# Kernel tuning notes

Measured on AMD Instinct MI355X. Metric: run time of the kernel, lower is better.

## Reference

```python
import jax, jax.numpy as jnp
import numpy as np

S, D, H, MLP = 2048, 1024, 16, 4096
DK = D // H
EPS = 1e-5  # torch LayerNorm default


def setup_inputs() -> dict:
    key = jax.random.key(0)
    ks = jax.random.split(key, 8)
    init = lambda k, shape, fan_in: jax.random.normal(k, shape, jnp.float32) * (fan_in ** -0.5)
    return {
        "x": jax.random.normal(ks[0], (S, D), jnp.float32),
        "wq": init(ks[1], (D, D), D), "bq": jnp.zeros((D,), jnp.float32),
        "wk": init(ks[2], (D, D), D), "bk": jnp.zeros((D,), jnp.float32),
        "wv": init(ks[3], (D, D), D), "bv": jnp.zeros((D,), jnp.float32),
        "wo": init(ks[4], (D, D), D), "bo": jnp.zeros((D,), jnp.float32),
        "w1": init(ks[5], (D, MLP), D), "b1": jnp.zeros((MLP,), jnp.float32),
        "w2": init(ks[6], (MLP, D), MLP), "b2": jnp.zeros((D,), jnp.float32),
        "ln1_g": jnp.ones((D,), jnp.float32), "ln1_b": jnp.zeros((D,), jnp.float32),
        "ln2_g": jnp.ones((D,), jnp.float32), "ln2_b": jnp.zeros((D,), jnp.float32),
    }


def _layernorm(x, g, b):
    m = jnp.mean(x, axis=-1, keepdims=True)
    v = jnp.var(x, axis=-1, keepdims=True)
    return (x - m) * jax.lax.rsqrt(v + EPS) * g + b


def reference(x, wq, bq, wk, bk, wv, bv, wo, bo, w1, b1, w2, b2, ln1_g, ln1_b, ln2_g, ln2_b):
    # --- residual 1: pre-LN multi-head self-attention ---
    h = _layernorm(x, ln1_g, ln1_b)
    q = (h @ wq + bq).reshape(S, H, DK).transpose(1, 0, 2)  # [H,S,DK]
    k = (h @ wk + bk).reshape(S, H, DK).transpose(1, 0, 2)
    v = (h @ wv + bv).reshape(S, H, DK).transpose(1, 0, 2)
    scores = jnp.einsum('hqd,hkd->hqk', q, k) / jnp.sqrt(jnp.float32(DK))  # [H,S,S]
    attn = jax.nn.softmax(scores, axis=-1)
    o = jnp.einsum('hqk,hkd->hqd', attn, v)  # [H,S,DK]
    # Faithful to original: x.contiguous().view(S, -1) is a raw reshape of the
    # [H,S,DK] buffer (no transpose back to [S,H,DK]).
    o = o.reshape(S, D)
    x = x + (o @ wo + bo)
    # --- residual 2: pre-LN GELU FFN ---
    h2 = _layernorm(x, ln2_g, ln2_b)
    f = jax.nn.gelu(h2 @ w1 + b1, approximate=False)  # torch nn.GELU = exact erf
    x = x + (f @ w2 + b2)
    return x
```

## Files before the change

kernel.cpp:

```cpp
#include <hip/hip_runtime.h>


constexpr int kS = 2048, kD = 1024, kH = 16, kDK = 64, kMLP = 4096;
constexpr float kEps = 1e-5f;

using u16 = unsigned short;
using u32 = unsigned int;
typedef float f32x4 __attribute__((ext_vector_type(4)));
typedef short bf16x8 __attribute__((ext_vector_type(8)));

__device__ __forceinline__ u16 f2b(float f) {
  u32 u = __builtin_bit_cast(u32, f);
  return (u16)((u + 0x7fffu + ((u >> 16) & 1u)) >> 16);
}

typedef const __attribute__((address_space(1))) u32* gas1;
typedef __attribute__((address_space(3))) u32* las3;
__device__ __forceinline__ void async16(const void* g, void* l) {
  __builtin_amdgcn_global_load_lds((gas1)g, (las3)l, 16, 0, 0);
}

__global__ __launch_bounds__(256)
void ln_kernel(const float* __restrict__ x, const float* __restrict__ g,
               const float* __restrict__ b, u16* __restrict__ out) {
  __shared__ float red[8];
  const int row = blockIdx.x, tid = threadIdx.x;
  const float4 v = *(const float4*)(x + (size_t)row * kD + tid * 4);
  float s = v.x + v.y + v.z + v.w;
  float ss = v.x * v.x + v.y * v.y + v.z * v.z + v.w * v.w;
#pragma unroll
  for (int d = 1; d < 64; d <<= 1) { s += __shfl_xor(s, d); ss += __shfl_xor(ss, d); }
  if ((tid & 63) == 0) { red[tid >> 6] = s; red[4 + (tid >> 6)] = ss; }
  __syncthreads();
  const float m = (red[0] + red[1] + red[2] + red[3]) * (1.f / kD);
  const float var = (red[4] + red[5] + red[6] + red[7]) * (1.f / kD) - m * m;
  const float r = rsqrtf(var + kEps);
  const float4 gv = *(const float4*)(g + tid * 4);
  const float4 bv = *(const float4*)(b + tid * 4);
  ushort4 o;
  o.x = f2b((v.x - m) * r * gv.x + bv.x);
  o.y = f2b((v.y - m) * r * gv.y + bv.y);
  o.z = f2b((v.z - m) * r * gv.z + bv.z);
  o.w = f2b((v.w - m) * r * gv.w + bv.w);
  *(ushort4*)(out + (size_t)row * kD + tid * 4) = o;
}

__global__ __launch_bounds__(256)
void transpose_cvt(const float* __restrict__ in, u16* __restrict__ out, int R, int C) {
  __shared__ float tile[32][33];
  const int c0 = blockIdx.x * 32, r0 = blockIdx.y * 32;
  const int x = threadIdx.x, y = threadIdx.y;
#pragma unroll
  for (int i = 0; i < 4; ++i)
    tile[y + i * 8][x] = in[(size_t)(r0 + y + i * 8) * C + c0 + x];
  __syncthreads();
#pragma unroll
  for (int i = 0; i < 4; ++i)
    out[(size_t)(c0 + y + i * 8) * R + r0 + x] = f2b(tile[x][y + i * 8]);
}

__global__ void concat_bias(const float* __restrict__ bq, const float* __restrict__ bk,
                            const float* __restrict__ bv, float* __restrict__ out) {
  int i = blockIdx.x * 256 + threadIdx.x;
  out[i] = i < kD ? bq[i] : (i < 2 * kD ? bk[i - kD] : bv[i - 2 * kD]);
}

__global__ __launch_bounds__(256)
void vtrans(const u16* __restrict__ qkv, u16* __restrict__ vt) {
  __shared__ u16 t[64][72];
  const int s0 = blockIdx.x * 64, h = blockIdx.y, tid = threadIdx.x;
#pragma unroll
  for (int r = 0; r < 2; ++r) {
    int chunk = r * 256 + tid, row = chunk >> 3, col = (chunk & 7) * 8;
    uint4 v = *(const uint4*)(qkv + (size_t)(s0 + row) * 3072 + 2 * kD + h * 64 + col);
    *(uint4*)(&t[row][col]) = v;
  }
  __syncthreads();
#pragma unroll
  for (int r = 0; r < 2; ++r) {
    int chunk = r * 256 + tid, drow = chunk >> 3, scol = (chunk & 7) * 8;
    u16 tmp[8];
#pragma unroll
    for (int j = 0; j < 8; ++j) tmp[j] = t[scol + j][drow];
    *(uint4*)(vt + (size_t)h * 64 * kS + (size_t)drow * kS + s0 + scol) = *(uint4*)tmp;
  }
}

template <int EPI>
__global__ __launch_bounds__(256, 2)
void gemm_bt(const u16* __restrict__ A, const u16* __restrict__ Bt,
             const float* __restrict__ bias, void* __restrict__ Cout,
             int N, int K, int Ksub) {
  constexpr int BM = 128, BN = 128, BK = 32;
  constexpr int MT = 4, NT = 4;
  __shared__ u16 As[BM * BK];
  __shared__ u16 Bs[BN * BK];
  const int tid = threadIdx.x;
  const int w = tid >> 6, l = tid & 63;
  const int wm = w >> 1, wn = w & 1;
  const int row0 = blockIdx.y * BM, col0 = blockIdx.x * BN;
  const int koff = blockIdx.z * Ksub;

  const int sc = ((l & 3) ^ ((l >> 3) & 3)) * 8;
  const u16* Ag = A + (size_t)(row0 + w * 16 + (l >> 2)) * K + koff + sc;
  const u16* Bg = Bt + (size_t)(col0 + w * 16 + (l >> 2)) * K + koff + sc;
  u16* AsW = As + w * 512;
  u16* BsW = Bs + w * 512;

  f32x4 acc[MT][NT] = {};
  const int q = l >> 4;

  for (int kt = 0; kt < Ksub; kt += BK) {
#pragma unroll
    for (int r = 0; r < 2; ++r) async16(Ag + (size_t)r * 64 * K + kt, AsW + r * 2048);
#pragma unroll
    for (int r = 0; r < 2; ++r) async16(Bg + (size_t)r * 64 * K + kt, BsW + r * 2048);
    __syncthreads();
    bf16x8 af[MT], bfr[NT];
#pragma unroll
    for (int i = 0; i < MT; ++i) {
      const int ra = wm * 64 + i * 16 + (l & 15);
      af[i] = *(const bf16x8*)(As + ra * 32 + (q ^ ((ra >> 1) & 3)) * 8);
    }
#pragma unroll
    for (int j = 0; j < NT; ++j) {
      const int rb = wn * 64 + j * 16 + (l & 15);
      bfr[j] = *(const bf16x8*)(Bs + rb * 32 + (q ^ ((rb >> 1) & 3)) * 8);
    }
#pragma unroll
    for (int i = 0; i < MT; ++i)
#pragma unroll
      for (int j = 0; j < NT; ++j)
        acc[i][j] = __builtin_amdgcn_mfma_f32_16x16x32_bf16(af[i], bfr[j], acc[i][j], 0, 0, 0);
    __syncthreads();
  }

  float* Pf = nullptr;
  if constexpr (EPI == 3)
    Pf = (float*)Cout + (size_t)blockIdx.z * gridDim.y * BM * N;
#pragma unroll
  for (int i = 0; i < MT; ++i) {
    const int row = row0 + wm * 64 + i * 16 + ((l >> 4) << 2);
#pragma unroll
    for (int j = 0; j < NT; ++j) {
      const int col = col0 + wn * 64 + j * 16 + (l & 15);
      float bb = 0.f;
      if constexpr (EPI != 3) bb = bias[col];
#pragma unroll
      for (int r = 0; r < 4; ++r) {
        const size_t idx = (size_t)(row + r) * N + col;
        float v = acc[i][j][r] + bb;
        if constexpr (EPI == 0) {
          ((u16*)Cout)[idx] = f2b(v);
        } else if constexpr (EPI == 1) {
          ((u16*)Cout)[idx] = f2b(0.5f * v * (1.f + erff(v * 0.7071067811865475f)));
        } else {
          Pf[idx] = v;
        }
      }
    }
  }
}

template <int KS>
__global__ __launch_bounds__(256)
void reduce_add(const float* __restrict__ parts, const float* __restrict__ bias,
                const float* __restrict__ res, float* __restrict__ out,
                int N, size_t strideMN) {
  const size_t b = ((size_t)blockIdx.x * 256 + threadIdx.x) * 4;
  float4 a = *(const float4*)(res + b);
  const float4 bv = *(const float4*)(bias + (b & (size_t)(N - 1)));
  a.x += bv.x; a.y += bv.y; a.z += bv.z; a.w += bv.w;
#pragma unroll
  for (int s = 0; s < KS; ++s) {
    const float4 p = *(const float4*)(parts + s * strideMN + b);
    a.x += p.x; a.y += p.y; a.z += p.z; a.w += p.w;
  }
  *(float4*)(out + b) = a;
}

__global__ __launch_bounds__(256, 3)
void flash_attn(const u16* __restrict__ qkv, const u16* __restrict__ vt,
                float* __restrict__ Op, float* __restrict__ Ml) {
  constexpr int LQ = 72;
  constexpr int LV = 136;
  constexpr int LP = 140;
  __shared__ u16 PsQ[4 * 16 * LP];
  __shared__ u16 Ks[128 * LQ];
  __shared__ u16 Vs[64 * LV];
  const int tid = threadIdx.x, w = tid >> 6, l = tid & 63;
  const int h = blockIdx.y, q0 = blockIdx.x * 64, z = blockIdx.z;
  const int kt0 = z * (kS / 2);

  const u16* Kg = qkv + kD + h * 64;
  const u16* Vg = vt + (size_t)h * 64 * kS;

  uint4 kreg[4], vreg[4];
  auto load_tile = [&](int kt) {
#pragma unroll
    for (int r = 0; r < 4; ++r) {
      int c = r * 256 + tid;
      kreg[r] = *(const uint4*)(Kg + (size_t)(kt + (c >> 3)) * 3072 + (c & 7) * 8);
    }
#pragma unroll
    for (int r = 0; r < 4; ++r) {
      int c = r * 256 + tid;
      vreg[r] = *(const uint4*)(Vg + (size_t)(c >> 4) * kS + kt + (c & 15) * 8);
    }
  };
  auto store_tile = [&]() {
#pragma unroll
    for (int r = 0; r < 4; ++r) {
      int c = r * 256 + tid;
      *(uint4*)(&Ks[(c >> 3) * LQ + (c & 7) * 8]) = kreg[r];
    }
#pragma unroll
    for (int r = 0; r < 4; ++r) {
      int c = r * 256 + tid;
      *(uint4*)(&Vs[(c >> 4) * LV + (c & 15) * 8]) = vreg[r];
    }
  };

#pragma unroll
  for (int r = 0; r < 2; ++r) {
    int c = r * 256 + tid;
    uint4 v = *(const uint4*)(qkv + (size_t)(q0 + (c >> 3)) * 3072 + h * 64 + (c & 7) * 8);
    *(uint4*)(&PsQ[(c >> 3) * LQ + (c & 7) * 8]) = v;
  }
  load_tile(kt0);
  __syncthreads();
  bf16x8 qa[2];
#pragma unroll
  for (int kq = 0; kq < 2; ++kq)
    qa[kq] = *(const bf16x8*)(&PsQ[(w * 16 + (l & 15)) * LQ + kq * 32 + (l >> 4) * 8]);
  u16* Ps = PsQ + w * 16 * LP;

  f32x4 oacc[4] = {};
  float mi[4], li[4];
#pragma unroll
  for (int r = 0; r < 4; ++r) { mi[r] = -1e30f; li[r] = 0.f; }

  for (int it = 0; it < 8; ++it) {
    store_tile();
    __syncthreads();
    if (it < 7) load_tile(kt0 + (it + 1) * 128);

    f32x4 s[8];
#pragma unroll
    for (int n = 0; n < 8; ++n) {
      f32x4 zz = {};
      bf16x8 kb0 = *(const bf16x8*)(&Ks[(n * 16 + (l & 15)) * LQ + (l >> 4) * 8]);
      bf16x8 kb1 = *(const bf16x8*)(&Ks[(n * 16 + (l & 15)) * LQ + 32 + (l >> 4) * 8]);
      zz = __builtin_amdgcn_mfma_f32_16x16x32_bf16(qa[0], kb0, zz, 0, 0, 0);
      zz = __builtin_amdgcn_mfma_f32_16x16x32_bf16(qa[1], kb1, zz, 0, 0, 0);
      s[n] = zz;
    }
    float alpha[4];
#pragma unroll
    for (int r = 0; r < 4; ++r) {
      float m = -1e30f;
#pragma unroll
      for (int n = 0; n < 8; ++n) m = fmaxf(m, s[n][r]);
#pragma unroll
      for (int d = 1; d < 16; d <<= 1) m = fmaxf(m, __shfl_xor(m, d));
      m *= 0.125f;
      float mn = fmaxf(mi[r], m);
      alpha[r] = __expf(mi[r] - mn);
      mi[r] = mn;
      li[r] *= alpha[r];
    }
#pragma unroll
    for (int n = 0; n < 4; ++n)
#pragma unroll
      for (int r = 0; r < 4; ++r) oacc[n][r] *= alpha[r];
    float rs[4] = {0.f, 0.f, 0.f, 0.f};
#pragma unroll
    for (int n = 0; n < 8; ++n)
#pragma unroll
      for (int r = 0; r < 4; ++r) {
        float pv = __expf(s[n][r] * 0.125f - mi[r]);
        rs[r] += pv;
        Ps[((l >> 4) * 4 + r) * LP + n * 16 + (l & 15)] = f2b(pv);
      }
#pragma unroll
    for (int r = 0; r < 4; ++r) {
      float t = rs[r];
#pragma unroll
      for (int d = 1; d < 16; d <<= 1) t += __shfl_xor(t, d);
      li[r] += t;
    }
    bf16x8 pa[4];
#pragma unroll
    for (int ks = 0; ks < 4; ++ks)
      pa[ks] = *(const bf16x8*)(&Ps[(l & 15) * LP + ks * 32 + (l >> 4) * 8]);
#pragma unroll
    for (int n = 0; n < 4; ++n)
#pragma unroll
      for (int ks = 0; ks < 4; ++ks) {
        bf16x8 vb = *(const bf16x8*)(&Vs[(n * 16 + (l & 15)) * LV + ks * 32 + (l >> 4) * 8]);
        oacc[n] = __builtin_amdgcn_mfma_f32_16x16x32_bf16(pa[ks], vb, oacc[n], 0, 0, 0);
      }
    __syncthreads();
  }

#pragma unroll
  for (int r = 0; r < 4; ++r) {
    const int srow = q0 + w * 16 + (l >> 4) * 4 + r;
    const size_t rowIdx = (size_t)(z * kH + h) * kS + srow;
    if ((l & 15) == 0) { Ml[rowIdx * 2] = mi[r]; Ml[rowIdx * 2 + 1] = li[r]; }
#pragma unroll
    for (int n = 0; n < 4; ++n)
      Op[rowIdx * kDK + n * 16 + (l & 15)] = oacc[n][r];
  }
}

__global__ __launch_bounds__(256)
void flash_combine(const float* __restrict__ Op, const float* __restrict__ Ml,
                   u16* __restrict__ og) {
  constexpr size_t HS = (size_t)kH * kS;
  constexpr size_t ZO = HS * kDK;
  const int t = blockIdx.x * 256 + threadIdx.x;
  const int d4 = (t & 15) * 4;
  const size_t row = (size_t)(t >> 4);
  const float m0 = Ml[row * 2], l0 = Ml[row * 2 + 1];
  const float m1 = Ml[(HS + row) * 2], l1 = Ml[(HS + row) * 2 + 1];
  const float m = fmaxf(m0, m1);
  const float w0 = __expf(m0 - m), w1 = __expf(m1 - m);
  const float inv = 1.f / (w0 * l0 + w1 * l1);
  const float4 a = *(const float4*)(Op + row * kDK + d4);
  const float4 b = *(const float4*)(Op + ZO + row * kDK + d4);
  ushort4 o;
  o.x = f2b((w0 * a.x + w1 * b.x) * inv);
  o.y = f2b((w0 * a.y + w1 * b.y) * inv);
  o.z = f2b((w0 * a.z + w1 * b.z) * inv);
  o.w = f2b((w0 * a.w + w1 * b.w) * inv);
  *(ushort4*)(og + row * kDK + d4) = o;
}

extern "C" void kernel_launch(void* const* d_in, const int* in_sizes, int n_in,
                              void* d_out, int out_size, void* d_ws, size_t ws_size,
                              hipStream_t stream) {
  const float* x = (const float*)d_in[0];
  const float* wq = (const float*)d_in[1];
  const float* bq = (const float*)d_in[2];
  const float* wk = (const float*)d_in[3];
  const float* bk = (const float*)d_in[4];
  const float* wv = (const float*)d_in[5];
  const float* bv = (const float*)d_in[6];
  const float* wo = (const float*)d_in[7];
  const float* bo = (const float*)d_in[8];
  const float* w1 = (const float*)d_in[9];
  const float* b1 = (const float*)d_in[10];
  const float* w2 = (const float*)d_in[11];
  const float* b2 = (const float*)d_in[12];
  const float* ln1g = (const float*)d_in[13];
  const float* ln1b = (const float*)d_in[14];
  const float* ln2g = (const float*)d_in[15];
  const float* ln2b = (const float*)d_in[16];
  float* out = (float*)d_out;

  char* p = (char*)d_ws;
  auto alloc = [&](size_t bytes) { void* q = (void*)p; p += (bytes + 255) & ~(size_t)255; return q; };
  u16* h1 = (u16*)alloc((size_t)kS * kD * 2);
  u16* wqkvt = (u16*)alloc((size_t)3 * kD * kD * 2);
  u16* qkv = (u16*)alloc((size_t)kS * 3 * kD * 2);
  u16* vt = (u16*)alloc((size_t)kH * kDK * kS * 2);
  u16* og = (u16*)alloc((size_t)kS * kD * 2);
  u16* wot = (u16*)alloc((size_t)kD * kD * 2);
  u16* h2 = (u16*)alloc((size_t)kS * kD * 2);
  u16* w1t = (u16*)alloc((size_t)kD * kMLP * 2);
  float* bqkv = (float*)alloc((size_t)3 * kD * 4);
  float* x2 = (float*)alloc((size_t)kS * kD * 4);
  u16* fbuf = (u16*)alloc((size_t)kS * kMLP * 2);
  u16* w2t = (u16*)alloc((size_t)kMLP * kD * 2);
  float* part = (float*)d_ws;
  float* Op = x2;
  float* Ml = Op + (size_t)2 * kH * kS * kDK;
  const size_t strideMN = (size_t)kS * kD;

  dim3 tb(32, 8);
  transpose_cvt<<<dim3(kD / 32, kD / 32), tb, 0, stream>>>(wq, wqkvt, kD, kD);
  transpose_cvt<<<dim3(kD / 32, kD / 32), tb, 0, stream>>>(wk, wqkvt + kD * kD, kD, kD);
  transpose_cvt<<<dim3(kD / 32, kD / 32), tb, 0, stream>>>(wv, wqkvt + 2 * kD * kD, kD, kD);
  transpose_cvt<<<dim3(kD / 32, kD / 32), tb, 0, stream>>>(wo, wot, kD, kD);
  transpose_cvt<<<dim3(kMLP / 32, kD / 32), tb, 0, stream>>>(w1, w1t, kD, kMLP);
  transpose_cvt<<<dim3(kD / 32, kMLP / 32), tb, 0, stream>>>(w2, w2t, kMLP, kD);
  concat_bias<<<dim3(12), dim3(256), 0, stream>>>(bq, bk, bv, bqkv);

  ln_kernel<<<dim3(kS), dim3(256), 0, stream>>>(x, ln1g, ln1b, h1);
  gemm_bt<0><<<dim3(3 * kD / 128, kS / 128, 1), dim3(256), 0, stream>>>(
      h1, wqkvt, bqkv, qkv, 3 * kD, kD, kD);
  vtrans<<<dim3(kS / 64, kH), dim3(256), 0, stream>>>(qkv, vt);
  flash_attn<<<dim3(kS / 64, kH, 2), dim3(256), 0, stream>>>(qkv, vt, Op, Ml);
  flash_combine<<<dim3(kH * kS * 16 / 256), dim3(256), 0, stream>>>(Op, Ml, og);
  gemm_bt<3><<<dim3(kD / 128, kS / 128, 2), dim3(256), 0, stream>>>(
      og, wot, nullptr, part, kD, kD, kD / 2);
  reduce_add<2><<<dim3(kS * kD / 4 / 256), dim3(256), 0, stream>>>(
      part, bo, x, x2, kD, strideMN);
  ln_kernel<<<dim3(kS), dim3(256), 0, stream>>>(x2, ln2g, ln2b, h2);
  gemm_bt<1><<<dim3(kMLP / 128, kS / 128, 1), dim3(256), 0, stream>>>(
      h2, w1t, b1, fbuf, kMLP, kD, kD);
  gemm_bt<3><<<dim3(kD / 128, kS / 128, 4), dim3(256), 0, stream>>>(
      fbuf, w2t, nullptr, part, kD, kMLP, kMLP / 4);
  reduce_add<4><<<dim3(kS * kD / 4 / 256), dim3(256), 0, stream>>>(
      part, b2, x2, out, kD, strideMN);
}
```

Before: 368.9 us.

## Load flash-attention Q/K/V tiles via async global-to-LDS with XOR swizzle

Replaces the register-staged K/V prefetch (global load into registers, then store to padded LDS) with direct global_load_lds async copies into unpadded LDS tiles, using an XOR swizzle on the 16-byte chunk index to avoid bank conflicts. This frees the registers that held the prefetch and drops the occupancy hint from launch bounds. The cost is losing software overlap: each iteration now issues the loads and waits at a barrier before computing, so load latency is exposed unless other resident waves hide it.

```diff
diff --git a/kernel.cpp b/kernel.cpp
--- a/kernel.cpp
+++ b/kernel.cpp
@@ -179,60 +179,36 @@
   *(float4*)(out + b) = a;
 }
 
-__global__ __launch_bounds__(256, 3)
+__global__ __launch_bounds__(256)
 void flash_attn(const u16* __restrict__ qkv, const u16* __restrict__ vt,
                 float* __restrict__ Op, float* __restrict__ Ml) {
-  constexpr int LQ = 72;
-  constexpr int LV = 136;
   constexpr int LP = 140;
   __shared__ u16 PsQ[4 * 16 * LP];
-  __shared__ u16 Ks[128 * LQ];
-  __shared__ u16 Vs[64 * LV];
+  __shared__ u16 Ks[128 * 64];
+  __shared__ u16 Vs[64 * 128];
   const int tid = threadIdx.x, w = tid >> 6, l = tid & 63;
   const int h = blockIdx.y, q0 = blockIdx.x * 64, z = blockIdx.z;
   const int kt0 = z * (kS / 2);
-
+  const int q = l >> 4;
+
+  const u16* Qg = qkv + h * 64;
   const u16* Kg = qkv + kD + h * 64;
   const u16* Vg = vt + (size_t)h * 64 * kS;
 
-  uint4 kreg[4], vreg[4];
-  auto load_tile = [&](int kt) {
-#pragma unroll
-    for (int r = 0; r < 4; ++r) {
-      int c = r * 256 + tid;
-      kreg[r] = *(const uint4*)(Kg + (size_t)(kt + (c >> 3)) * 3072 + (c & 7) * 8);
-    }
-#pragma unroll
-    for (int r = 0; r < 4; ++r) {
-      int c = r * 256 + tid;
-      vreg[r] = *(const uint4*)(Vg + (size_t)(c >> 4) * kS + kt + (c & 15) * 8);
-    }
-  };
-  auto store_tile = [&]() {
-#pragma unroll
-    for (int r = 0; r < 4; ++r) {
-      int c = r * 256 + tid;
-      *(uint4*)(&Ks[(c >> 3) * LQ + (c & 7) * 8]) = kreg[r];
-    }
-#pragma unroll
-    for (int r = 0; r < 4; ++r) {
-      int c = r * 256 + tid;
-      *(uint4*)(&Vs[(c >> 4) * LV + (c & 15) * 8]) = vreg[r];
-    }
-  };
-
-#pragma unroll
-  for (int r = 0; r < 2; ++r) {
-    int c = r * 256 + tid;
-    uint4 v = *(const uint4*)(qkv + (size_t)(q0 + (c >> 3)) * 3072 + h * 64 + (c & 7) * 8);
-    *(uint4*)(&PsQ[(c >> 3) * LQ + (c & 7) * 8]) = v;
-  }
-  load_tile(kt0);
+  {
+    const int r8 = l >> 3, c = (l & 7) ^ r8;
+#pragma unroll
+    for (int p = 0; p < 2; ++p) {
+      const int row = (p * 4 + w) * 8 + r8;
+      async16(Qg + (size_t)(q0 + row) * 3072 + c * 8, PsQ + (p * 4 + w) * 512);
+    }
+  }
   __syncthreads();
   bf16x8 qa[2];
+  const int rq = w * 16 + (l & 15);
 #pragma unroll
   for (int kq = 0; kq < 2; ++kq)
-    qa[kq] = *(const bf16x8*)(&PsQ[(w * 16 + (l & 15)) * LQ + kq * 32 + (l >> 4) * 8]);
+    qa[kq] = *(const bf16x8*)(PsQ + rq * 64 + ((kq * 4 + q) ^ (l & 7)) * 8);
   u16* Ps = PsQ + w * 16 * LP;
 
   f32x4 oacc[4] = {};
@@ -241,16 +217,33 @@
   for (int r = 0; r < 4; ++r) { mi[r] = -1e30f; li[r] = 0.f; }
 
   for (int it = 0; it < 8; ++it) {
-    store_tile();
     __syncthreads();
-    if (it < 7) load_tile(kt0 + (it + 1) * 128);
+    const int kt = kt0 + it * 128;
+    {
+      const int r8 = l >> 3, c = (l & 7) ^ r8;
+#pragma unroll
+      for (int p = 0; p < 4; ++p) {
+        const int row = (p * 4 + w) * 8 + r8;
+        async16(Kg + (size_t)(kt + row) * 3072 + c * 8, Ks + (p * 4 + w) * 512);
+      }
+    }
+    {
+#pragma unroll
+      for (int p = 0; p < 4; ++p) {
+        const int row = (p * 4 + w) * 4 + (l >> 4);
+        const int c = (l & 15) ^ (row & 7);
+        async16(Vg + (size_t)row * kS + kt + c * 8, Vs + (p * 4 + w) * 512);
+      }
+    }
+    __syncthreads();
 
     f32x4 s[8];
 #pragma unroll
     for (int n = 0; n < 8; ++n) {
+      const int rk = n * 16 + (l & 15);
       f32x4 zz = {};
-      bf16x8 kb0 = *(const bf16x8*)(&Ks[(n * 16 + (l & 15)) * LQ + (l >> 4) * 8]);
-      bf16x8 kb1 = *(const bf16x8*)(&Ks[(n * 16 + (l & 15)) * LQ + 32 + (l >> 4) * 8]);
+      bf16x8 kb0 = *(const bf16x8*)(Ks + rk * 64 + ((0 + q) ^ (rk & 7)) * 8);
+      bf16x8 kb1 = *(const bf16x8*)(Ks + rk * 64 + ((4 + q) ^ (rk & 7)) * 8);
       zz = __builtin_amdgcn_mfma_f32_16x16x32_bf16(qa[0], kb0, zz, 0, 0, 0);
       zz = __builtin_amdgcn_mfma_f32_16x16x32_bf16(qa[1], kb1, zz, 0, 0, 0);
       s[n] = zz;
@@ -292,15 +285,16 @@
     bf16x8 pa[4];
 #pragma unroll
     for (int ks = 0; ks < 4; ++ks)
-      pa[ks] = *(const bf16x8*)(&Ps[(l & 15) * LP + ks * 32 + (l >> 4) * 8]);
-#pragma unroll
-    for (int n = 0; n < 4; ++n)
+      pa[ks] = *(const bf16x8*)(&Ps[(l & 15) * LP + ks * 32 + q * 8]);
+#pragma unroll
+    for (int n = 0; n < 4; ++n) {
+      const int rv = n * 16 + (l & 15);
 #pragma unroll
       for (int ks = 0; ks < 4; ++ks) {
-        bf16x8 vb = *(const bf16x8*)(&Vs[(n * 16 + (l & 15)) * LV + ks * 32 + (l >> 4) * 8]);
+        bf16x8 vb = *(const bf16x8*)(Vs + rv * 128 + ((ks * 4 + q) ^ (rv & 7)) * 8);
         oacc[n] = __builtin_amdgcn_mfma_f32_16x16x32_bf16(pa[ks], vb, oacc[n], 0, 0, 0);
       }
-    __syncthreads();
+    }
   }
 
 #pragma unroll
```

New measurement: 332.2 us. 9.9% less time.
